# Kernel tuning notes

Hardware: AMD Instinct MI355X
Metric: run time of the kernel (lower is better)

The kernel has to match this reference:

```python
import jax, jax.numpy as jnp
import numpy as np

N_SECTIONS = 4  # cascaded biquads (direct-form II transposed), 2 states each


def setup_inputs() -> dict:
    key = jax.random.key(0)
    k1, k2, k3 = jax.random.split(key, 3)
    B, T = 512, 32768
    x = jax.random.normal(k1, (B, T, 1), dtype=jnp.float32)
    # scale coefficients so the IIR recurrence stays stable over T steps
    b = jax.random.normal(k2, (N_SECTIONS, 3), dtype=jnp.float32) * 0.5
    a = jax.random.normal(k3, (N_SECTIONS, 2), dtype=jnp.float32) * 0.1
    return {"x": x, "b": b, "a": a}


def reference(x, b, a):
    # x: (B, T, 1) -> per-step scalar signal per batch element.
    # Cascade of N_SECTIONS biquads, direct-form II transposed:
    #   y  = b0*u + s1
    #   s1' = b1*u - a1*y + s2
    #   s2' = b2*u - a2*y
    B = x.shape[0]
    xs = x[..., 0].T  # (T, B): scan over time, vectorized over batch
    init_states = jnp.zeros((N_SECTIONS, 2, B), dtype=x.dtype)

    def step(states, u_t):
        sig = u_t  # (B,)
        new_states = []
        for k in range(N_SECTIONS):  # fixed small structural loop
            s1, s2 = states[k, 0], states[k, 1]
            y = b[k, 0] * sig + s1
            ns1 = b[k, 1] * sig - a[k, 0] * y + s2
            ns2 = b[k, 2] * sig - a[k, 1] * y
            new_states.append(jnp.stack([ns1, ns2]))
            sig = y
        return jnp.stack(new_states), sig

    _, ys = jax.lax.scan(step, init_states, xs)  # ys: (T, B)
    return ys.T[..., None]  # (B, T, 1), matching out_sequence.unsqueeze(-1)
```

## Files before the change

### kernel.cpp

```cpp
#include <hip/hip_runtime.h>


namespace {
constexpr int NS     = 4;
constexpr int BATCH  = 512;
constexpr int TLEN   = 32768;
constexpr int NSTATE = 8;
constexpr int P      = 512;
constexpr int L      = TLEN / P;
constexpr int LQ     = L / 4;
constexpr int LOG2P  = 9;
constexpr int LOG2L  = 6;
constexpr int NSQ    = LOG2L + LOG2P - 1;
}

#if defined(__has_builtin)
#  if __has_builtin(__builtin_amdgcn_global_load_lds)
#    define USE_GLL 1
#  endif
#endif
#ifndef USE_GLL
#  define USE_GLL 0
#endif

#define WAIT_VM0 do { asm volatile("s_waitcnt vmcnt(0)" ::: "memory"); \
                      __builtin_amdgcn_sched_barrier(0); } while (0)
#define WAIT_LGKM0 do { asm volatile("s_waitcnt lgkmcnt(0)" ::: "memory"); \
                        __builtin_amdgcn_sched_barrier(0); } while (0)

__device__ __forceinline__ void load_coefs(const float* __restrict__ bc,
                                           const float* __restrict__ ac,
                                           float b0[NS], float b1[NS], float b2[NS],
                                           float a1[NS], float a2[NS]) {
#pragma unroll
  for (int k = 0; k < NS; ++k) {
    b0[k] = bc[3 * k];
    b1[k] = bc[3 * k + 1];
    b2[k] = bc[3 * k + 2];
    a1[k] = ac[2 * k];
    a2[k] = ac[2 * k + 1];
  }
}

__device__ __forceinline__ float step_cascade(float sig,
                                              const float b0[NS], const float b1[NS],
                                              const float b2[NS], const float a1[NS],
                                              const float a2[NS],
                                              float s1[NS], float s2[NS]) {
#pragma unroll
  for (int k = 0; k < NS; ++k) {
    float y = fmaf(b0[k], sig, s1[k]);
    s1[k]   = fmaf(-a1[k], y, fmaf(b1[k], sig, s2[k]));
    s2[k]   = fmaf(-a2[k], y, b2[k] * sig);
    sig = y;
  }
  return sig;
}

#define CO b0, b1, b2, a1, a2

__device__ __forceinline__ void adv4(const float4 u,
                                     const float b0[NS], const float b1[NS],
                                     const float b2[NS], const float a1[NS],
                                     const float a2[NS], float s1[NS], float s2[NS]) {
  (void)step_cascade(u.x, CO, s1, s2);
  (void)step_cascade(u.y, CO, s1, s2);
  (void)step_cascade(u.z, CO, s1, s2);
  (void)step_cascade(u.w, CO, s1, s2);
}

__device__ __forceinline__ float4 out4(const float4 u,
                                       const float b0[NS], const float b1[NS],
                                       const float b2[NS], const float a1[NS],
                                       const float a2[NS], float s1[NS], float s2[NS]) {
  float4 y;
  y.x = step_cascade(u.x, CO, s1, s2);
  y.y = step_cascade(u.y, CO, s1, s2);
  y.z = step_cascade(u.z, CO, s1, s2);
  y.w = step_cascade(u.w, CO, s1, s2);
  return y;
}

__device__ __forceinline__ void stage_ht(const float4* __restrict__ gx_w,
                                         float4* R, int lane, int ht) {
#if USE_GLL
#pragma unroll
  for (int j = 0; j < 8; ++j) {
    const int cc = j * 8 + (lane >> 3);
    const int qq = lane & 7;
    const float4* g = gx_w + cc * 16 + ht * 8 + (qq ^ (cc & 7));
    __builtin_amdgcn_global_load_lds(
        (const __attribute__((address_space(1))) void*)g,
        (__attribute__((address_space(3))) void*)&R[j * 64], 16, 0, 0);
  }
#else
#pragma unroll
  for (int j = 0; j < 8; ++j) {
    const int cc = j * 8 + (lane >> 3);
    const int qq = lane & 7;
    R[j * 64 + lane] = gx_w[cc * 16 + ht * 8 + (qq ^ (cc & 7))];
  }
#endif
}

__global__ __launch_bounds__(P) void k_fused(const float* __restrict__ x,
                                             const float* __restrict__ bc,
                                             const float* __restrict__ ac,
                                             float* __restrict__ out) {
  __shared__ float4 arena[4096];
  float* Msf = reinterpret_cast<float*>(arena);
  float* Wf  = reinterpret_cast<float*>(arena) + 576;

  const int t    = threadIdx.x;
  const int lane = t & 63;
  const int wv   = t >> 6;
  const int swz  = lane & 7;
  float4* __restrict__ R = arena + (wv << 9);

  float b0[NS], b1[NS], b2[NS], a1[NS], a2[NS];
  load_coefs(bc, ac, b0, b1, b2, a1, a2);

  const float4* __restrict__ gx_w = reinterpret_cast<const float4*>(x) +
      (size_t)blockIdx.x * (P * LQ) + ((size_t)wv << 10);
  float4* __restrict__ gy_w = reinterpret_cast<float4*>(out) +
      (size_t)blockIdx.x * (P * LQ) + ((size_t)wv << 10);

  stage_ht(gx_w, R, lane, 0);

  float mpow[9];
#pragma unroll
  for (int i = 0; i < 9; ++i) mpow[i] = 0.0f;
  if (t < 64) {
    const int r = lane >> 3, c = lane & 7;
    float p1[NS] = {0.f, 0.f, 0.f, 0.f};
    float p2[NS] = {0.f, 0.f, 0.f, 0.f};
    if (c & 1) p2[c >> 1] = 1.0f; else p1[c >> 1] = 1.0f;
    (void)step_cascade(0.0f, CO, p1, p2);
    float m = (r & 1) ? p2[r >> 1] : p1[r >> 1];
#pragma unroll
    for (int it = 0; it < NSQ; ++it) {
      float acc = 0.0f;
#pragma unroll
      for (int k = 0; k < NSTATE; ++k)
        acc = fmaf(__shfl(m, r * 8 + k), __shfl(m, k * 8 + c), acc);
      m = acc;
      if (it >= LOG2L - 1) mpow[it - (LOG2L - 1)] = m;
    }
  }

  float s1[NS] = {0.f, 0.f, 0.f, 0.f};
  float s2[NS] = {0.f, 0.f, 0.f, 0.f};
  WAIT_VM0;
#pragma unroll
  for (int q = 0; q < 8; ++q) adv4(R[lane * 8 + (q ^ swz)], CO, s1, s2);
  WAIT_LGKM0;
  stage_ht(gx_w, R, lane, 1);
  WAIT_VM0;
#pragma unroll
  for (int q = 0; q < 8; ++q) adv4(R[lane * 8 + (q ^ swz)], CO, s1, s2);

  float w[NSTATE];
#pragma unroll
  for (int k = 0; k < NS; ++k) { w[2 * k] = s1[k]; w[2 * k + 1] = s2[k]; }

  __syncthreads();
  if (t < 64) {
#pragma unroll
    for (int d = 0; d < LOG2P; ++d) Msf[d * 64 + t] = mpow[d];
  }

  for (int d = 0; d < LOG2P; ++d) {
#pragma unroll
    for (int r = 0; r < NSTATE; ++r) Wf[t * 9 + r] = w[r];
    __syncthreads();
    if (t >= (1 << d)) {
      const int src = (t - (1 << d)) * 9;
      float prev[NSTATE];
#pragma unroll
      for (int r = 0; r < NSTATE; ++r) prev[r] = Wf[src + r];
#pragma unroll
      for (int r = 0; r < NSTATE; ++r) {
        float acc = w[r];
#pragma unroll
        for (int k = 0; k < NSTATE; ++k)
          acc = fmaf(Msf[d * 64 + r * 8 + k], prev[k], acc);
        w[r] = acc;
      }
    }
    __syncthreads();
  }

#pragma unroll
  for (int r = 0; r < NSTATE; ++r) Wf[t * 9 + r] = w[r];
  __syncthreads();
  {
    const int src = (t == 0 ? 0 : t - 1) * 9;
#pragma unroll
    for (int k = 0; k < NS; ++k) {
      s1[k] = (t == 0) ? 0.0f : Wf[src + 2 * k];
      s2[k] = (t == 0) ? 0.0f : Wf[src + 2 * k + 1];
    }
  }
  __syncthreads();

#pragma unroll
  for (int ht = 0; ht < 2; ++ht) {
    stage_ht(gx_w, R, lane, ht);
    WAIT_VM0;
#pragma unroll
    for (int q = 0; q < 8; ++q) {
      const int s = lane * 8 + (q ^ swz);
      R[s] = out4(R[s], CO, s1, s2);
    }
    WAIT_LGKM0;
#pragma unroll
    for (int j = 0; j < 8; ++j) {
      const int cc = j * 8 + (lane >> 3);
      const int qq = lane & 7;
      const float4 v = R[j * 64 + lane];
      gy_w[cc * 16 + ht * 8 + (qq ^ (cc & 7))] = v;
    }
    if (ht == 0) WAIT_LGKM0;
  }
}

extern "C" void kernel_launch(void* const* d_in, const int* in_sizes, int n_in,
                              void* d_out, int out_size, void* d_ws, size_t ws_size,
                              hipStream_t stream) {
  const float* x  = (const float*)d_in[0];
  const float* bc = (const float*)d_in[1];
  const float* ac = (const float*)d_in[2];
  float* out = (float*)d_out;

  k_fused<<<BATCH, P, 0, stream>>>(x, bc, ac, out);
}
```

Baseline: 41.48 us.

## Replace block-wide Hillis-Steele state scan with wave-shuffle scan plus cross-wave carry

The block-level prefix scan of 8-state carries, which used shared memory with two barriers per level over nine levels, becomes a six-level intra-wave shuffle scan. A single barrier exchanges per-wave boundary states, and each wave serially composes the preceding waves' carries and then applies per-lane matrix powers selected by lane bits. Every wave now computes its own matrix powers redundantly. The x reload for the first half is issued before the scan, and the second-half load overlaps the first-half stores via a partial vmcnt wait. This trades extra per-thread FMAs for far fewer block barriers.

```diff
diff --git a/kernel.cpp b/kernel.cpp
--- a/kernel.cpp
+++ b/kernel.cpp
@@ -9,9 +9,7 @@
 constexpr int P      = 512;
 constexpr int L      = TLEN / P;
 constexpr int LQ     = L / 4;
-constexpr int LOG2P  = 9;
-constexpr int LOG2L  = 6;
-constexpr int NSQ    = LOG2L + LOG2P - 1;
+constexpr int NMS    = 7;
 }
 
 #if defined(__has_builtin)
@@ -24,6 +22,8 @@
 #endif
 
 #define WAIT_VM0 do { asm volatile("s_waitcnt vmcnt(0)" ::: "memory"); \
+                      __builtin_amdgcn_sched_barrier(0); } while (0)
+#define WAIT_VM8 do { asm volatile("s_waitcnt vmcnt(8)" ::: "memory"); \
                       __builtin_amdgcn_sched_barrier(0); } while (0)
 #define WAIT_LGKM0 do { asm volatile("s_waitcnt lgkmcnt(0)" ::: "memory"); \
                         __builtin_amdgcn_sched_barrier(0); } while (0)
@@ -108,8 +108,8 @@
                                              const float* __restrict__ ac,
                                              float* __restrict__ out) {
   __shared__ float4 arena[4096];
-  float* Msf = reinterpret_cast<float*>(arena);
-  float* Wf  = reinterpret_cast<float*>(arena) + 576;
+  __shared__ float  Msw[8][NMS][64];
+  __shared__ float  Bnd[8][8];
 
   const int t    = threadIdx.x;
   const int lane = t & 63;
@@ -127,10 +127,7 @@
 
   stage_ht(gx_w, R, lane, 0);
 
-  float mpow[9];
-#pragma unroll
-  for (int i = 0; i < 9; ++i) mpow[i] = 0.0f;
-  if (t < 64) {
+  {
     const int r = lane >> 3, c = lane & 7;
     float p1[NS] = {0.f, 0.f, 0.f, 0.f};
     float p2[NS] = {0.f, 0.f, 0.f, 0.f};
@@ -138,13 +135,13 @@
     (void)step_cascade(0.0f, CO, p1, p2);
     float m = (r & 1) ? p2[r >> 1] : p1[r >> 1];
 #pragma unroll
-    for (int it = 0; it < NSQ; ++it) {
+    for (int it = 0; it < 12; ++it) {
       float acc = 0.0f;
 #pragma unroll
       for (int k = 0; k < NSTATE; ++k)
         acc = fmaf(__shfl(m, r * 8 + k), __shfl(m, k * 8 + c), acc);
       m = acc;
-      if (it >= LOG2L - 1) mpow[it - (LOG2L - 1)] = m;
+      if (it >= 5) Msw[wv][it - 5][lane] = m;
     }
   }
 
@@ -163,64 +160,112 @@
 #pragma unroll
   for (int k = 0; k < NS; ++k) { w[2 * k] = s1[k]; w[2 * k + 1] = s2[k]; }
 
-  __syncthreads();
-  if (t < 64) {
-#pragma unroll
-    for (int d = 0; d < LOG2P; ++d) Msf[d * 64 + t] = mpow[d];
-  }
-
-  for (int d = 0; d < LOG2P; ++d) {
-#pragma unroll
-    for (int r = 0; r < NSTATE; ++r) Wf[t * 9 + r] = w[r];
-    __syncthreads();
-    if (t >= (1 << d)) {
-      const int src = (t - (1 << d)) * 9;
-      float prev[NSTATE];
-#pragma unroll
-      for (int r = 0; r < NSTATE; ++r) prev[r] = Wf[src + r];
+  WAIT_LGKM0;
+  stage_ht(gx_w, R, lane, 0);
+
+#pragma unroll
+  for (int d = 0; d < 6; ++d) {
+    const int off = 1 << d;
+    const int src = (lane >= off) ? (lane - off) : lane;
+    float prev[NSTATE];
+#pragma unroll
+    for (int r = 0; r < NSTATE; ++r) prev[r] = __shfl(w[r], src);
+    if (lane >= off) {
 #pragma unroll
       for (int r = 0; r < NSTATE; ++r) {
         float acc = w[r];
 #pragma unroll
         for (int k = 0; k < NSTATE; ++k)
-          acc = fmaf(Msf[d * 64 + r * 8 + k], prev[k], acc);
+          acc = fmaf(Msw[wv][d][r * 8 + k], prev[k], acc);
         w[r] = acc;
       }
     }
-    __syncthreads();
-  }
-
-#pragma unroll
-  for (int r = 0; r < NSTATE; ++r) Wf[t * 9 + r] = w[r];
-  __syncthreads();
+  }
+
+  if (lane == 63) {
+#pragma unroll
+    for (int r = 0; r < NSTATE; ++r) Bnd[wv][r] = w[r];
+  }
+  asm volatile("s_waitcnt lgkmcnt(0)" ::: "memory");
+  __builtin_amdgcn_s_barrier();
+
+  float Pv[NSTATE] = {0.f, 0.f, 0.f, 0.f, 0.f, 0.f, 0.f, 0.f};
+  for (int j = 0; j < wv; ++j) {
+    float np[NSTATE];
+#pragma unroll
+    for (int r = 0; r < NSTATE; ++r) {
+      float acc = Bnd[j][r];
+#pragma unroll
+      for (int k = 0; k < NSTATE; ++k)
+        acc = fmaf(Msw[wv][6][r * 8 + k], Pv[k], acc);
+      np[r] = acc;
+    }
+#pragma unroll
+    for (int r = 0; r < NSTATE; ++r) Pv[r] = np[r];
+  }
+
+  float z[NSTATE];
+#pragma unroll
+  for (int r = 0; r < NSTATE; ++r) z[r] = Pv[r];
+#pragma unroll
+  for (int b = 0; b < 6; ++b) {
+    float zb[NSTATE];
+#pragma unroll
+    for (int r = 0; r < NSTATE; ++r) {
+      float acc = 0.0f;
+#pragma unroll
+      for (int k = 0; k < NSTATE; ++k)
+        acc = fmaf(Msw[wv][b][r * 8 + k], z[k], acc);
+      zb[r] = acc;
+    }
+    const bool bit = (lane >> b) & 1;
+#pragma unroll
+    for (int r = 0; r < NSTATE; ++r) z[r] = bit ? zb[r] : z[r];
+  }
   {
-    const int src = (t == 0 ? 0 : t - 1) * 9;
+    const int esrc = lane ? lane - 1 : 0;
 #pragma unroll
     for (int k = 0; k < NS; ++k) {
-      s1[k] = (t == 0) ? 0.0f : Wf[src + 2 * k];
-      s2[k] = (t == 0) ? 0.0f : Wf[src + 2 * k + 1];
-    }
-  }
-  __syncthreads();
-
-#pragma unroll
-  for (int ht = 0; ht < 2; ++ht) {
-    stage_ht(gx_w, R, lane, ht);
-    WAIT_VM0;
-#pragma unroll
-    for (int q = 0; q < 8; ++q) {
-      const int s = lane * 8 + (q ^ swz);
-      R[s] = out4(R[s], CO, s1, s2);
-    }
-    WAIT_LGKM0;
-#pragma unroll
-    for (int j = 0; j < 8; ++j) {
-      const int cc = j * 8 + (lane >> 3);
-      const int qq = lane & 7;
-      const float4 v = R[j * 64 + lane];
-      gy_w[cc * 16 + ht * 8 + (qq ^ (cc & 7))] = v;
-    }
-    if (ht == 0) WAIT_LGKM0;
+      const float ue0 = __shfl(w[2 * k], esrc);
+      const float ue1 = __shfl(w[2 * k + 1], esrc);
+      s1[k] = (lane ? ue0 : 0.0f) + z[2 * k];
+      s2[k] = (lane ? ue1 : 0.0f) + z[2 * k + 1];
+    }
+  }
+
+  WAIT_VM0;
+#pragma unroll
+  for (int q = 0; q < 8; ++q) {
+    const int s = lane * 8 + (q ^ swz);
+    R[s] = out4(R[s], CO, s1, s2);
+  }
+  WAIT_LGKM0;
+  float4 v[8];
+#pragma unroll
+  for (int j = 0; j < 8; ++j) v[j] = R[j * 64 + lane];
+  WAIT_LGKM0;
+  stage_ht(gx_w, R, lane, 1);
+#pragma unroll
+  for (int j = 0; j < 8; ++j) {
+    const int cc = j * 8 + (lane >> 3);
+    const int qq = lane & 7;
+    gy_w[cc * 16 + (qq ^ (cc & 7))] = v[j];
+  }
+  WAIT_VM8;
+#pragma unroll
+  for (int q = 0; q < 8; ++q) {
+    const int s = lane * 8 + (q ^ swz);
+    R[s] = out4(R[s], CO, s1, s2);
+  }
+  WAIT_LGKM0;
+#pragma unroll
+  for (int j = 0; j < 8; ++j) v[j] = R[j * 64 + lane];
+  WAIT_LGKM0;
+#pragma unroll
+  for (int j = 0; j < 8; ++j) {
+    const int cc = j * 8 + (lane >> 3);
+    const int qq = lane & 7;
+    gy_w[cc * 16 + 8 + (qq ^ (cc & 7))] = v[j];
   }
 }
 
```

Result: slower. 70.62 us (+70.3%).
